# Kernel tuning notes

Measured on AMD Instinct MI355X. Metric: run time of the kernel, lower is better.

Reference implementation:

```python
import jax, jax.numpy as jnp
import numpy as np

B, C, H, W, Q = 4, 64, 128, 128, 65536
HID, OUT = 256, 3
IN_DIM = C + 4  # q_feat (C) + rel coord (2) + cell (2)


def setup_inputs() -> dict:
    key = jax.random.key(0)
    ks = jax.random.split(key, 16)
    feat = jax.random.normal(ks[0], (B, C, H, W), dtype=jnp.float32)
    s_grid = jax.random.uniform(ks[1], (B, Q, 2), dtype=jnp.float32, minval=-1.0, maxval=1.0)
    # cell size of a 256x256 output image in [-1,1] coords: 2/256 per axis
    s_cell = jnp.full((B, Q, 2), 2.0 / 256.0, dtype=jnp.float32)
    dims = [IN_DIM, HID, HID, HID, HID, OUT]
    inp = {"feat": feat, "s_grid": s_grid, "s_cell": s_cell}
    for i in range(5):
        inp[f"w{i}"] = 0.02 * jax.random.normal(ks[2 + 2 * i], (dims[i], dims[i + 1]), dtype=jnp.float32)
        inp[f"b{i}"] = jnp.zeros((dims[i + 1],), dtype=jnp.float32)
    return inp


def reference(feat, s_grid, s_cell, w0, b0, w1, b1, w2, b2, w3, b3, w4, b4):
    Bf, Cf, Hf, Wf = feat.shape
    eps = 1e-6
    dh, dw = 1.0 / Hf, 1.0 / Wf
    dt = feat.dtype
    # q_cell scaled by feature resolution
    qc = s_cell * jnp.asarray([Hf, Wf], dtype=dt)  # [B,Q,2]
    feat_flat = feat.reshape(Bf, Cf, Hf * Wf)
    ws, bs = [w0, w1, w2, w3], [b0, b1, b2, b3]

    preds, areas = [], []
    for r in (-1.0, 1.0):
        for c in (-1.0, 1.0):
            # shifted, clamped query grid (channel 0 = h/y, channel 1 = w/x)
            gy = jnp.clip(s_grid[..., 0] + r * dh, -1.0 + eps, 1.0 - eps)
            gx = jnp.clip(s_grid[..., 1] + c * dw, -1.0 + eps, 1.0 - eps)
            # grid_sample nearest, align_corners=False: unnormalize then round (half-even, as nearbyint)
            iy = jnp.clip(jnp.round(((gy + 1.0) * Hf - 1.0) * 0.5).astype(jnp.int32), 0, Hf - 1)
            ix = jnp.clip(jnp.round(((gx + 1.0) * Wf - 1.0) * 0.5).astype(jnp.int32), 0, Wf - 1)
            lin = iy * Wf + ix  # [B,Q]
            q_feat = jnp.take_along_axis(feat_flat, lin[:, None, :], axis=2).transpose(0, 2, 1)  # [B,Q,C]
            # coord of the gathered pixel center (= grid_sample of make_coord feat_grid)
            py = -1.0 + (2.0 * iy.astype(dt) + 1.0) / Hf
            px = -1.0 + (2.0 * ix.astype(dt) + 1.0) / Wf
            rel_y = (s_grid[..., 0] - py) * Hf
            rel_x = (s_grid[..., 1] - px) * Wf
            rel = jnp.stack([rel_y, rel_x], axis=-1)  # [B,Q,2]
            h = jnp.concatenate([q_feat, rel, qc], axis=-1)  # [B,Q,C+4]
            for wl, bl in zip(ws, bs):
                h = jax.nn.relu(h @ wl + bl)
            pred = h @ w4 + b4  # [B,Q,OUT]
            preds.append(pred)
            areas.append(jnp.abs(rel_y * rel_x) + 1e-9)

    total = areas[0] + areas[1] + areas[2] + areas[3]
    # LIIF swaps diagonally-opposite areas: 0<->3, 1<->2
    areas = [areas[3], areas[2], areas[1], areas[0]]
    ret = preds[0] * (areas[0] / total)[..., None]
    for p, a in zip(preds[1:], areas[1:]):
        ret = ret + p * (a / total)[..., None]
    return ret
```

## Files before the change

kernel.cpp:

```cpp
#include <hip/hip_runtime.h>


typedef _Float16 half8 __attribute__((ext_vector_type(8)));
typedef float f32x4 __attribute__((ext_vector_type(4)));

#define ROWS     256
#define THREADS  1024

#define A_BYTES    131072
#define AREA_OFF   131072
#define PRED_OFF   132096
#define FLAG_OFF   136192
#define SMEM_BYTES 136224

static __device__ __forceinline__ unsigned short f2h(float f) {
    union { _Float16 h; unsigned short u; } v;
    v.h = (_Float16)f;
    return v.u;
}

#define SWZ(row, byte) ((byte) ^ (((row) & 7) << 4))

static __device__ __host__ __forceinline__ int PI(int p) {
    return ((p >> 6) << 6) | ((p & 15) << 2) | ((p >> 4) & 3);
}

__global__ void transpose_feat(const float* __restrict__ feat,
                               unsigned short* __restrict__ featT) {
    __shared__ float tile[64][65];
    const int bi  = blockIdx.x;
    const int b   = bi >> 8;
    const int rem = bi & 255;
    const int y   = rem >> 1;
    const int xc  = (rem & 1) << 6;
    const int tid = threadIdx.x;

    {
        const int x  = tid & 63;
        const int cg = tid >> 6;
#pragma unroll
        for (int i = 0; i < 16; ++i) {
            int c = cg * 16 + i;
            tile[c][x] = feat[(((b << 6) + c) << 14) + (y << 7) + xc + x];
        }
    }
    __syncthreads();
    {
        const int c  = tid & 63;
        const int xg = tid >> 6;
#pragma unroll
        for (int i = 0; i < 16; ++i) {
            int xx = xg * 16 + i;
            featT[(size_t)((((b << 7) + y) << 7) + xc + xx) * 64 + c] =
                f2h(tile[c][xx]);
        }
    }
}

__global__ void pack_w(const float* __restrict__ src,
                       unsigned short* __restrict__ dst,
                       int K, int N, int ksteps, int nct, int permN) {
    int tid = blockIdx.x * 256 + threadIdx.x;
    int total = ksteps * nct * 512;
    if (tid >= total) return;
    int j    = tid & 7;
    int lane = (tid >> 3) & 63;
    int f    = tid >> 9;
    int ct   = f % nct;
    int ks   = f / nct;
    int k = ks * 32 + ((lane >> 4) << 3) + j;
    int n = ct * 16 + (lane & 15);
    int ns = permN ? PI(n) : n;
    float v = (k < K && ns < N) ? src[k * N + ns] : 0.0f;
    dst[tid] = f2h(v);
}

template <int NP>
static __device__ __forceinline__ void layer_step(
    char* A, int* rflag, int* wflag, int target,
    const unsigned short* __restrict__ wsel,
    const float* __restrict__ bsel,
    int lane, int wm, int wn) {

    const int l15 = lane & 15;
    f32x4 acc[4][4];
#pragma unroll
    for (int rf = 0; rf < 4; ++rf)
#pragma unroll
        for (int cf = 0; cf < 4; ++cf)
            acc[rf][cf] = (f32x4){0.f, 0.f, 0.f, 0.f};

#pragma unroll 2
    for (int kp = 0; kp < NP; ++kp) {
        half8 af[4], bf[4];
        const int kbyte = (kp << 6) + ((lane >> 4) << 4);
        const int xorv  = (lane & 7) << 4;
#pragma unroll
        for (int rf = 0; rf < 4; ++rf) {
            int row = wm * 64 + rf * 16 + l15;
            af[rf] = *(const half8*)(A + row * 512 + (kbyte ^ xorv));
        }
#pragma unroll
        for (int cf = 0; cf < 4; ++cf)
            bf[cf] = *(const half8*)(wsel + (size_t)((kp * 16 + wn * 4 + cf) * 64 + lane) * 8);
        __builtin_amdgcn_s_setprio(1);
#pragma unroll
        for (int rf = 0; rf < 4; ++rf)
#pragma unroll
            for (int cf = 0; cf < 4; ++cf)
                acc[rf][cf] = __builtin_amdgcn_mfma_f32_16x16x32_f16(
                    af[rf], bf[cf], acc[rf][cf], 0, 0, 0);
        __builtin_amdgcn_s_setprio(0);
    }

    if (lane == 0)
        __hip_atomic_fetch_add(rflag, 1, __ATOMIC_RELEASE,
                               __HIP_MEMORY_SCOPE_WORKGROUP);
    while (__hip_atomic_load(rflag, __ATOMIC_ACQUIRE,
                             __HIP_MEMORY_SCOPE_WORKGROUP) < target)
        __builtin_amdgcn_s_sleep(4);

    const float4 bias = *(const float4*)(bsel + wn * 64 + l15 * 4);
    const int colbyte = (wn << 7) + (l15 << 3);

#pragma unroll
    for (int rf = 0; rf < 4; ++rf) {
        const int rbase = wm * 64 + rf * 16 + ((lane >> 4) << 2);
#pragma unroll
        for (int q = 0; q < 4; ++q) {
            const int row = rbase + q;
            union { _Float16 h[4]; uint2 u; } pk;
            pk.h[0] = (_Float16)fmaxf(acc[rf][0][q] + bias.x, 0.0f);
            pk.h[1] = (_Float16)fmaxf(acc[rf][1][q] + bias.y, 0.0f);
            pk.h[2] = (_Float16)fmaxf(acc[rf][2][q] + bias.z, 0.0f);
            pk.h[3] = (_Float16)fmaxf(acc[rf][3][q] + bias.w, 0.0f);
            *(uint2*)(A + row * 512 + (colbyte ^ ((row & 7) << 4))) = pk.u;
        }
    }

    if (lane == 0)
        __hip_atomic_fetch_add(wflag, 1, __ATOMIC_RELEASE,
                               __HIP_MEMORY_SCOPE_WORKGROUP);
    while (__hip_atomic_load(wflag, __ATOMIC_ACQUIRE,
                             __HIP_MEMORY_SCOPE_WORKGROUP) < target)
        __builtin_amdgcn_s_sleep(4);
}

__global__ __launch_bounds__(1024, 4) void mlp_main(
    const unsigned short* __restrict__ featT,
    const float* __restrict__ sgrid,
    const float* __restrict__ scell,
    const unsigned short* __restrict__ wp0, const unsigned short* __restrict__ wp1,
    const unsigned short* __restrict__ wp2, const unsigned short* __restrict__ wp3,
    const unsigned short* __restrict__ wp4,
    const float* __restrict__ bp0, const float* __restrict__ bp1,
    const float* __restrict__ bp2, const float* __restrict__ bp3,
    const float* __restrict__ bp4,
    float* __restrict__ out) {

    extern __shared__ char lds[];
    char*  A     = lds;
    float* areas = (float*)(lds + AREA_OFF);
    float* predl = (float*)(lds + PRED_OFF);
    int*   flags = (int*)(lds + FLAG_OFF);

    const int tid  = threadIdx.x;
    const int lane = tid & 63;
    const int wv   = tid >> 6;
    const int wm   = wv >> 2;
    const int wn   = wv & 3;

    if (tid < 8) flags[tid] = 0;

    if (tid < 512) {
        const int row  = tid >> 1;
        const int half = tid & 1;
        const int grow = blockIdx.x * ROWS + row;
        const int qq   = grow >> 2;
        const int s    = grow & 3;
        const int b    = qq >> 16;

        const float g0 = sgrid[qq * 2 + 0];
        const float g1 = sgrid[qq * 2 + 1];
        const float c0 = scell[qq * 2 + 0];
        const float c1 = scell[qq * 2 + 1];

        const float rs = (s & 2) ? 1.0f : -1.0f;
        const float cs = (s & 1) ? 1.0f : -1.0f;
        const float dh = 0.0078125f;
        const float LO = (float)(-1.0 + 1e-6);
        const float HI = (float)( 1.0 - 1e-6);

        float gy = fminf(fmaxf(g0 + rs * dh, LO), HI);
        float gx = fminf(fmaxf(g1 + cs * dh, LO), HI);
        float ty = ((gy + 1.0f) * 128.0f - 1.0f) * 0.5f;
        float tx = ((gx + 1.0f) * 128.0f - 1.0f) * 0.5f;
        int iy = (int)rintf(ty); iy = min(max(iy, 0), 127);
        int ix = (int)rintf(tx); ix = min(max(ix, 0), 127);

        float py = -1.0f + (float)(2 * iy + 1) * 0.0078125f;
        float px = -1.0f + (float)(2 * ix + 1) * 0.0078125f;
        float rel_y = (g0 - py) * 128.0f;
        float rel_x = (g1 - px) * 128.0f;
        float qcy = c0 * 128.0f;
        float qcx = c1 * 128.0f;

        if (half == 0) areas[row] = fabsf(rel_y * rel_x) + 1e-9f;

        const unsigned short* src =
            featT + (size_t)((((b << 7) + iy) << 7) + ix) * 64 + (half << 5);
        uint4 v0 = *(const uint4*)(src + 0);
        uint4 v1 = *(const uint4*)(src + 8);
        uint4 v2 = *(const uint4*)(src + 16);
        uint4 v3 = *(const uint4*)(src + 24);

        char* arow = A + row * 512;
        const int kb0 = half << 6;
        *(uint4*)(arow + SWZ(row, kb0 +  0)) = v0;
        *(uint4*)(arow + SWZ(row, kb0 + 16)) = v1;
        *(uint4*)(arow + SWZ(row, kb0 + 32)) = v2;
        *(uint4*)(arow + SWZ(row, kb0 + 48)) = v3;

        if (half) {
            uint4 t;
            t.x = (unsigned)f2h(rel_y) | ((unsigned)f2h(rel_x) << 16);
            t.y = (unsigned)f2h(qcy)   | ((unsigned)f2h(qcx)   << 16);
            t.z = 0; t.w = 0;
            uint4 z = {0, 0, 0, 0};
            *(uint4*)(arow + SWZ(row, 128)) = t;
            *(uint4*)(arow + SWZ(row, 144)) = z;
            *(uint4*)(arow + SWZ(row, 160)) = z;
            *(uint4*)(arow + SWZ(row, 176)) = z;
        }
    }
    __syncthreads();

    int* rflag = &flags[wm];
    int* wflag = &flags[4 + wm];
    layer_step<3>(A, rflag, wflag,  4, wp0, bp0, lane, wm, wn);
    layer_step<8>(A, rflag, wflag,  8, wp1, bp1, lane, wm, wn);
    layer_step<8>(A, rflag, wflag, 12, wp2, bp2, lane, wm, wn);
    layer_step<8>(A, rflag, wflag, 16, wp3, bp3, lane, wm, wn);

    {
        f32x4 a4 = (f32x4){0.f, 0.f, 0.f, 0.f};
        const int xorv = (lane & 7) << 4;
#pragma unroll
        for (int kp = 0; kp < 8; ++kp) {
            const int kbyte = (kp << 6) + ((lane >> 4) << 4);
            half8 b = *(const half8*)(wp4 + (size_t)((kp * 64) + lane) * 8);
            int row = wv * 16 + (lane & 15);
            half8 a = *(const half8*)(A + row * 512 + (kbyte ^ xorv));
            a4 = __builtin_amdgcn_mfma_f32_16x16x32_f16(a, b, a4, 0, 0, 0);
        }

        const int col = lane & 15;
        const float b4v = (col < 3) ? bp4[col] : 0.0f;
        if (col < 3) {
#pragma unroll
            for (int q = 0; q < 4; ++q) {
                int row = wv * 16 + ((lane >> 4) << 2) + q;
                predl[row * 4 + col] = a4[q] + b4v;
            }
        }
        __syncthreads();

        if (tid < 192) {
            int qloc = tid / 3;
            int c    = tid - qloc * 3;
            int r0   = qloc * 4;
            float a0 = areas[r0 + 0], a1 = areas[r0 + 1];
            float a2 = areas[r0 + 2], a3 = areas[r0 + 3];
            float total = ((a0 + a1) + a2) + a3;
            float ret = predl[(r0 + 0) * 4 + c] * (a3 / total);
            ret      += predl[(r0 + 1) * 4 + c] * (a2 / total);
            ret      += predl[(r0 + 2) * 4 + c] * (a1 / total);
            ret      += predl[(r0 + 3) * 4 + c] * (a0 / total);
            int qq0 = blockIdx.x * 64 + qloc;
            out[qq0 * 3 + c] = ret;
        }
    }
}

extern "C" void kernel_launch(void* const* d_in, const int* in_sizes, int n_in,
                              void* d_out, int out_size, void* d_ws, size_t ws_size,
                              hipStream_t stream) {
    const float* feat  = (const float*)d_in[0];
    const float* sgrid = (const float*)d_in[1];
    const float* scell = (const float*)d_in[2];
    const float* w0 = (const float*)d_in[3];
    const float* b0 = (const float*)d_in[4];
    const float* w1 = (const float*)d_in[5];
    const float* b1 = (const float*)d_in[6];
    const float* w2 = (const float*)d_in[7];
    const float* b2 = (const float*)d_in[8];
    const float* w3 = (const float*)d_in[9];
    const float* b3 = (const float*)d_in[10];
    const float* w4 = (const float*)d_in[11];
    const float* b4 = (const float*)d_in[12];

    char* ws = (char*)d_ws;
    unsigned short* featT = (unsigned short*)ws;
    unsigned short* wp0 = (unsigned short*)(ws + 8388608);
    unsigned short* wp1 = (unsigned short*)(ws + 8388608 + 49152);
    unsigned short* wp2 = (unsigned short*)(ws + 8388608 + 49152 + 131072);
    unsigned short* wp3 = (unsigned short*)(ws + 8388608 + 49152 + 2 * 131072);
    unsigned short* wp4 = (unsigned short*)(ws + 8388608 + 49152 + 3 * 131072);

    transpose_feat<<<1024, 256, 0, stream>>>(feat, featT);
    pack_w<<<96,  256, 0, stream>>>(w0, wp0,  68, 256, 3, 16, 1);
    pack_w<<<256, 256, 0, stream>>>(w1, wp1, 256, 256, 8, 16, 1);
    pack_w<<<256, 256, 0, stream>>>(w2, wp2, 256, 256, 8, 16, 1);
    pack_w<<<256, 256, 0, stream>>>(w3, wp3, 256, 256, 8, 16, 1);
    pack_w<<<16,  256, 0, stream>>>(w4, wp4, 256, 3, 8, 1, 0);

    hipFuncSetAttribute(reinterpret_cast<const void*>(mlp_main),
                        hipFuncAttributeMaxDynamicSharedMemorySize, SMEM_BYTES);
    mlp_main<<<4096, THREADS, SMEM_BYTES, stream>>>(
        featT, sgrid, scell, wp0, wp1, wp2, wp3, wp4,
        b0, b1, b2, b3, b4, (float*)d_out);
}
```

Before: 448.0 us.

## Halve block to 512 threads with 64x128 per-wave MLP tiles

```diff
diff --git a/kernel.cpp b/kernel.cpp
--- a/kernel.cpp
+++ b/kernel.cpp
@@ -5,7 +5,7 @@
 typedef float f32x4 __attribute__((ext_vector_type(4)));
 
 #define ROWS     256
-#define THREADS  1024
+#define THREADS  512
 
 #define A_BYTES    131072
 #define AREA_OFF   131072
@@ -83,16 +83,16 @@
     int lane, int wm, int wn) {
 
     const int l15 = lane & 15;
-    f32x4 acc[4][4];
+    f32x4 acc[4][8];
 #pragma unroll
     for (int rf = 0; rf < 4; ++rf)
 #pragma unroll
-        for (int cf = 0; cf < 4; ++cf)
+        for (int cf = 0; cf < 8; ++cf)
             acc[rf][cf] = (f32x4){0.f, 0.f, 0.f, 0.f};
 
 #pragma unroll 2
     for (int kp = 0; kp < NP; ++kp) {
-        half8 af[4], bf[4];
+        half8 af[4], bf[8];
         const int kbyte = (kp << 6) + ((lane >> 4) << 4);
         const int xorv  = (lane & 7) << 4;
 #pragma unroll
@@ -101,13 +101,13 @@
             af[rf] = *(const half8*)(A + row * 512 + (kbyte ^ xorv));
         }
 #pragma unroll
-        for (int cf = 0; cf < 4; ++cf)
-            bf[cf] = *(const half8*)(wsel + (size_t)((kp * 16 + wn * 4 + cf) * 64 + lane) * 8);
+        for (int cf = 0; cf < 8; ++cf)
+            bf[cf] = *(const half8*)(wsel + (size_t)((kp * 16 + wn * 8 + cf) * 64 + lane) * 8);
         __builtin_amdgcn_s_setprio(1);
 #pragma unroll
         for (int rf = 0; rf < 4; ++rf)
 #pragma unroll
-            for (int cf = 0; cf < 4; ++cf)
+            for (int cf = 0; cf < 8; ++cf)
                 acc[rf][cf] = __builtin_amdgcn_mfma_f32_16x16x32_f16(
                     af[rf], bf[cf], acc[rf][cf], 0, 0, 0);
         __builtin_amdgcn_s_setprio(0);
@@ -120,8 +120,10 @@
                              __HIP_MEMORY_SCOPE_WORKGROUP) < target)
         __builtin_amdgcn_s_sleep(4);
 
-    const float4 bias = *(const float4*)(bsel + wn * 64 + l15 * 4);
-    const int colbyte = (wn << 7) + (l15 << 3);
+    const float4 biasA = *(const float4*)(bsel + wn * 128 + l15 * 4);
+    const float4 biasB = *(const float4*)(bsel + wn * 128 + 64 + l15 * 4);
+    const int colb0 = (wn << 8) + (l15 << 3);
+    const int colb1 = colb0 + 128;
 
 #pragma unroll
     for (int rf = 0; rf < 4; ++rf) {
@@ -129,12 +131,18 @@
 #pragma unroll
         for (int q = 0; q < 4; ++q) {
             const int row = rbase + q;
+            const int rx  = (row & 7) << 4;
             union { _Float16 h[4]; uint2 u; } pk;
-            pk.h[0] = (_Float16)fmaxf(acc[rf][0][q] + bias.x, 0.0f);
-            pk.h[1] = (_Float16)fmaxf(acc[rf][1][q] + bias.y, 0.0f);
-            pk.h[2] = (_Float16)fmaxf(acc[rf][2][q] + bias.z, 0.0f);
-            pk.h[3] = (_Float16)fmaxf(acc[rf][3][q] + bias.w, 0.0f);
-            *(uint2*)(A + row * 512 + (colbyte ^ ((row & 7) << 4))) = pk.u;
+            pk.h[0] = (_Float16)fmaxf(acc[rf][0][q] + biasA.x, 0.0f);
+            pk.h[1] = (_Float16)fmaxf(acc[rf][1][q] + biasA.y, 0.0f);
+            pk.h[2] = (_Float16)fmaxf(acc[rf][2][q] + biasA.z, 0.0f);
+            pk.h[3] = (_Float16)fmaxf(acc[rf][3][q] + biasA.w, 0.0f);
+            *(uint2*)(A + row * 512 + (colb0 ^ rx)) = pk.u;
+            pk.h[0] = (_Float16)fmaxf(acc[rf][4][q] + biasB.x, 0.0f);
+            pk.h[1] = (_Float16)fmaxf(acc[rf][5][q] + biasB.y, 0.0f);
+            pk.h[2] = (_Float16)fmaxf(acc[rf][6][q] + biasB.z, 0.0f);
+            pk.h[3] = (_Float16)fmaxf(acc[rf][7][q] + biasB.w, 0.0f);
+            *(uint2*)(A + row * 512 + (colb1 ^ rx)) = pk.u;
         }
     }
 
@@ -146,7 +154,7 @@
         __builtin_amdgcn_s_sleep(4);
 }
 
-__global__ __launch_bounds__(1024, 4) void mlp_main(
+__global__ __launch_bounds__(512, 2) void mlp_main(
     const unsigned short* __restrict__ featT,
     const float* __restrict__ sgrid,
     const float* __restrict__ scell,
@@ -167,12 +175,12 @@
     const int tid  = threadIdx.x;
     const int lane = tid & 63;
     const int wv   = tid >> 6;
-    const int wm   = wv >> 2;
-    const int wn   = wv & 3;
+    const int wm   = wv >> 1;
+    const int wn   = wv & 1;
 
     if (tid < 8) flags[tid] = 0;
 
-    if (tid < 512) {
+    {
         const int row  = tid >> 1;
         const int half = tid & 1;
         const int grow = blockIdx.x * ROWS + row;
@@ -237,31 +245,38 @@
 
     int* rflag = &flags[wm];
     int* wflag = &flags[4 + wm];
-    layer_step<3>(A, rflag, wflag,  4, wp0, bp0, lane, wm, wn);
-    layer_step<8>(A, rflag, wflag,  8, wp1, bp1, lane, wm, wn);
-    layer_step<8>(A, rflag, wflag, 12, wp2, bp2, lane, wm, wn);
-    layer_step<8>(A, rflag, wflag, 16, wp3, bp3, lane, wm, wn);
+    layer_step<3>(A, rflag, wflag, 2, wp0, bp0, lane, wm, wn);
+    layer_step<8>(A, rflag, wflag, 4, wp1, bp1, lane, wm, wn);
+    layer_step<8>(A, rflag, wflag, 6, wp2, bp2, lane, wm, wn);
+    layer_step<8>(A, rflag, wflag, 8, wp3, bp3, lane, wm, wn);
 
     {
-        f32x4 a4 = (f32x4){0.f, 0.f, 0.f, 0.f};
+        f32x4 a4[2];
+        a4[0] = (f32x4){0.f, 0.f, 0.f, 0.f};
+        a4[1] = (f32x4){0.f, 0.f, 0.f, 0.f};
         const int xorv = (lane & 7) << 4;
 #pragma unroll
         for (int kp = 0; kp < 8; ++kp) {
             const int kbyte = (kp << 6) + ((lane >> 4) << 4);
             half8 b = *(const half8*)(wp4 + (size_t)((kp * 64) + lane) * 8);
-            int row = wv * 16 + (lane & 15);
-            half8 a = *(const half8*)(A + row * 512 + (kbyte ^ xorv));
-            a4 = __builtin_amdgcn_mfma_f32_16x16x32_f16(a, b, a4, 0, 0, 0);
+#pragma unroll
+            for (int rr = 0; rr < 2; ++rr) {
+                int row = wv * 32 + rr * 16 + (lane & 15);
+                half8 a = *(const half8*)(A + row * 512 + (kbyte ^ xorv));
+                a4[rr] = __builtin_amdgcn_mfma_f32_16x16x32_f16(a, b, a4[rr], 0, 0, 0);
+            }
         }
 
         const int col = lane & 15;
         const float b4v = (col < 3) ? bp4[col] : 0.0f;
         if (col < 3) {
 #pragma unroll
-            for (int q = 0; q < 4; ++q) {
-                int row = wv * 16 + ((lane >> 4) << 2) + q;
-                predl[row * 4 + col] = a4[q] + b4v;
-            }
+            for (int rr = 0; rr < 2; ++rr)
+#pragma unroll
+                for (int q = 0; q < 4; ++q) {
+                    int row = wv * 32 + rr * 16 + ((lane >> 4) << 2) + q;
+                    predl[row * 4 + col] = a4[rr][q] + b4v;
+                }
         }
         __syncthreads();
 
```

Result: faster. 414.1 us (-7.6%).
